# Performance work log

Measured on AMD Instinct MI355X. Metric: run time of the kernel, lower is better.

## Reference

```python
import jax, jax.numpy as jnp
import numpy as np

B, D, H, L_NS, L_S_DIM = 8, 512, 8, 64, 2048
HEAD_DIM = D // H


def setup_inputs() -> dict:
    key = jax.random.key(0)
    ks = jax.random.split(key, 12)
    L = L_S_DIM + L_NS
    x = jax.random.normal(ks[0], (B, L, D), jnp.float32)
    padding_mask = jax.random.randint(ks[1], (B, L_S_DIM), 0, 2, jnp.int32)
    s = 0.02
    params = {}
    for idx, name in enumerate(['wq', 'wk', 'wv']):
        params[name + '_sw'] = jax.random.normal(ks[2 + 3 * idx], (D, D), jnp.float32) * s
        params[name + '_sb'] = jnp.zeros((D,), jnp.float32)
        params[name + '_nw'] = jax.random.normal(ks[3 + 3 * idx], (L_NS, D, D), jnp.float32) * s
        params[name + '_nb'] = jnp.zeros((L_NS, D), jnp.float32)
    params['out_w'] = jax.random.normal(ks[11], (D, D), jnp.float32) * s
    params['out_b'] = jnp.zeros((D,), jnp.float32)
    return dict(x=x, padding_mask=padding_mask, L_s=2048, L_s_out=512, **params)


def mix_linear(x, L_s, sw, sb, nw, nb):
    # shared projection for first L_s tokens, token-specific weights for the rest
    out_s = x[:, :L_s] @ sw + sb                                # [B, L_s, D]
    out_ns = jnp.einsum('bni,nio->bno', x[:, L_s:], nw) + nb    # [B, L_ns, D]
    return jnp.concatenate([out_s, out_ns], axis=1)


def reference(x, padding_mask, L_s, L_s_out,
              wq_sw, wq_sb, wq_nw, wq_nb,
              wk_sw, wk_sb, wk_nw, wk_nb,
              wv_sw, wv_sb, wv_nw, wv_nb,
              out_w, out_b):
    Bb, L, d = x.shape
    L_ns = wq_nw.shape[0]
    hd = d // H
    K = mix_linear(x, L_s, wk_sw, wk_sb, wk_nw, wk_nb).reshape(Bb, L, H, hd).transpose(0, 2, 1, 3)
    V = mix_linear(x, L_s, wv_sw, wv_sb, wv_nw, wv_nb).reshape(Bb, L, H, hd).transpose(0, 2, 1, 3)
    if L_s_out < L_s:
        q_input = jnp.concatenate([x[:, L_s - L_s_out:L_s], x[:, L_s:]], axis=1)
    else:
        q_input = x
    L_q = L_s_out + L_ns
    L_k = L_s + L_ns
    Q = mix_linear(q_input, L_s_out, wq_sw, wq_sb, wq_nw, wq_nb).reshape(Bb, L_q, H, hd).transpose(0, 2, 1, 3)
    scores = jnp.einsum('bhqd,bhkd->bhqk', Q, K) / jnp.asarray(np.sqrt(hd), jnp.float32)
    i = jnp.arange(L_q)[:, None]
    j = jnp.arange(L_k)[None, :]
    causal = j <= i + (L_k - L_q)                                # [L_q, L_k]
    pad = jnp.concatenate([padding_mask.astype(bool), jnp.ones((Bb, L_ns), bool)], axis=1)
    mask = causal[None, None] & pad[:, None, None, :]            # [B, 1, L_q, L_k]
    scores = jnp.where(mask, scores, -1e9)
    w = jax.nn.softmax(scores, axis=-1)
    out = jnp.einsum('bhqk,bhkd->bhqd', w, V).transpose(0, 2, 1, 3).reshape(Bb, L_q, d)
    return out @ out_w + out_b
```

## Files before the change

kernel.cpp:

```cpp
#include <hip/hip_runtime.h>

typedef unsigned short u16;
typedef unsigned long long u64;
typedef short bf16x8 __attribute__((ext_vector_type(8)));
typedef float f32x4 __attribute__((ext_vector_type(4)));
typedef unsigned short u16x8 __attribute__((ext_vector_type(8)));

#define ATT_C (0.125f * 1.44269504088896340736f)

__device__ __forceinline__ u16 f2bf(float f) {
  unsigned u = __builtin_bit_cast(unsigned int, f);
  u += 0x7FFFu + ((u >> 16) & 1u);
  return (u16)(u >> 16);
}
__device__ __forceinline__ float bf2f(u16 u) {
  return __builtin_bit_cast(float, (unsigned)u << 16);
}
__device__ __forceinline__ void gload_lds16(const void* g, void* l) {
  __builtin_amdgcn_global_load_lds((__attribute__((address_space(1))) void*)(void*)g,
                                   (__attribute__((address_space(3))) void*)l, 16, 0, 0);
}

__global__ __launch_bounds__(256) void k_prep_pm(const int* __restrict__ pmask, u64* __restrict__ pbits) {
  int b = blockIdx.x;
  int t = threadIdx.x, w = t >> 6, l = t & 63;
  #pragma unroll
  for (int i = 0; i < 8; ++i) {
    int tile = i * 4 + w;
    u64 m = __ballot(pmask[b * 2048 + tile * 64 + l] != 0);
    if (l == 0) pbits[b * 32 + tile] = m;
  }
}

__global__ __launch_bounds__(256) void k_prep_x(const float* __restrict__ x, u16* __restrict__ xb) {
  int i = blockIdx.x * 256 + threadIdx.x;
  float4 v = reinterpret_cast<const float4*>(x)[i];
  ushort4 o;
  o.x = f2bf(v.x); o.y = f2bf(v.y); o.z = f2bf(v.z); o.w = f2bf(v.w);
  reinterpret_cast<ushort4*>(xb)[i] = o;
}

__global__ __launch_bounds__(256) void k_prep_wt(const float* __restrict__ w0, const float* __restrict__ w1,
                                                 const float* __restrict__ w2, const float* __restrict__ w3,
                                                 u16* __restrict__ wt) {
  __shared__ float Tl[64][65];
  int z = blockIdx.y;
  const float* W = (z == 0) ? w0 : (z == 1) ? w1 : (z == 2) ? w2 : w3;
  int kt = blockIdx.x >> 3, nt = blockIdx.x & 7;
  int t = threadIdx.x;
  int c = (t & 15) * 4, r0 = t >> 4;
  #pragma unroll
  for (int p = 0; p < 4; ++p) {
    int r = r0 + p * 16;
    float4 v = *reinterpret_cast<const float4*>(&W[(kt * 64 + r) * 512 + nt * 64 + c]);
    Tl[r][c] = v.x; Tl[r][c + 1] = v.y; Tl[r][c + 2] = v.z; Tl[r][c + 3] = v.w;
  }
  __syncthreads();
  #pragma unroll
  for (int p = 0; p < 4; ++p) {
    int n = r0 + p * 16;
    ushort4 u;
    u.x = f2bf(Tl[c + 0][n]); u.y = f2bf(Tl[c + 1][n]);
    u.z = f2bf(Tl[c + 2][n]); u.w = f2bf(Tl[c + 3][n]);
    *reinterpret_cast<ushort4*>(&wt[(z << 18) + (nt * 64 + n) * 512 + kt * 64 + c]) = u;
  }
}

__global__ __launch_bounds__(256) void k_nonshared(
    const float* __restrict__ x,
    const float* __restrict__ wq_nw, const float* __restrict__ wq_nb,
    const float* __restrict__ wk_nw, const float* __restrict__ wk_nb,
    const float* __restrict__ wv_nw, const float* __restrict__ wv_nb,
    u16* __restrict__ Qp, u16* __restrict__ Kp, u16* __restrict__ Vt) {
  int n = blockIdx.x, p = blockIdx.y;
  const float* W  = (p == 0) ? wq_nw : (p == 1) ? wk_nw : wv_nw;
  const float* bb = (p == 0) ? wq_nb : (p == 1) ? wk_nb : wv_nb;
  W += (long)n * 262144; bb += n * 512;
  __shared__ float As[4096];
  int t = threadIdx.x;
  #pragma unroll
  for (int i = 0; i < 4; ++i) {
    int f4 = t + i * 256;
    int bi = f4 >> 7;
    int off = (f4 & 127) * 4;
    reinterpret_cast<float4*>(As)[f4] =
        *reinterpret_cast<const float4*>(&x[(bi * 2112 + 2048 + n) * 512 + off]);
  }
  __syncthreads();
  int c4 = (t & 127) * 4, ih = t >> 7;
  float acc[8][4];
  #pragma unroll
  for (int b2 = 0; b2 < 8; ++b2) { acc[b2][0]=0.f; acc[b2][1]=0.f; acc[b2][2]=0.f; acc[b2][3]=0.f; }
  int i0 = ih * 256;
  #pragma unroll 8
  for (int i = i0; i < i0 + 256; ++i) {
    float4 wr = *reinterpret_cast<const float4*>(&W[i * 512 + c4]);
    #pragma unroll
    for (int b2 = 0; b2 < 8; ++b2) {
      float a = As[b2 * 512 + i];
      acc[b2][0] += a * wr.x; acc[b2][1] += a * wr.y;
      acc[b2][2] += a * wr.z; acc[b2][3] += a * wr.w;
    }
  }
  __syncthreads();
  if (ih == 1) {
    #pragma unroll
    for (int b2 = 0; b2 < 8; ++b2)
      reinterpret_cast<float4*>(As)[(t & 127) * 8 + b2] =
          make_float4(acc[b2][0], acc[b2][1], acc[b2][2], acc[b2][3]);
  }
  __syncthreads();
  if (ih == 0) {
    float4 bv = *reinterpret_cast<const float4*>(&bb[c4]);
    #pragma unroll
    for (int b2 = 0; b2 < 8; ++b2) {
      float4 o2 = reinterpret_cast<float4*>(As)[(t & 127) * 8 + b2];
      float r0 = acc[b2][0] + o2.x + bv.x, r1 = acc[b2][1] + o2.y + bv.y;
      float r2 = acc[b2][2] + o2.z + bv.z, r3 = acc[b2][3] + o2.w + bv.w;
      if (p == 0) {
        ushort4 u; u.x = f2bf(r0); u.y = f2bf(r1); u.z = f2bf(r2); u.w = f2bf(r3);
        *reinterpret_cast<ushort4*>(&Qp[(b2 * 576 + 512 + n) * 512 + c4]) = u;
      } else if (p == 1) {
        ushort4 u; u.x = f2bf(r0); u.y = f2bf(r1); u.z = f2bf(r2); u.w = f2bf(r3);
        *reinterpret_cast<ushort4*>(&Kp[(b2 * 2112 + 2048 + n) * 512 + c4]) = u;
      } else {
        Vt[(b2 * 512 + c4 + 0) * 2112 + 2048 + n] = f2bf(r0);
        Vt[(b2 * 512 + c4 + 1) * 2112 + 2048 + n] = f2bf(r1);
        Vt[(b2 * 512 + c4 + 2) * 2112 + 2048 + n] = f2bf(r2);
        Vt[(b2 * 512 + c4 + 3) * 2112 + 2048 + n] = f2bf(r3);
      }
    }
  }
}

template<int AMODE, int CMODE>
__global__ __launch_bounds__(256) void k_gemm(const u16* __restrict__ A, const u16* __restrict__ Wt,
                                              const float* __restrict__ bias, void* __restrict__ Cp,
                                              int mtpb, int arowoff, int cbs) {
  __shared__ u16 Al[4096];
  __shared__ u16 Wl[4096];
  int t = threadIdx.x, w = t >> 6, l = t & 63;
  int bm = blockIdx.x, n0 = blockIdx.y << 7;
  int batch = bm / mtpb, mt = bm % mtpb;
  int rowbase = batch * 2112 + arowoff + mt * 128;
  f32x4 zero = {0.f, 0.f, 0.f, 0.f};
  f32x4 acc[4][4];
  #pragma unroll
  for (int i = 0; i < 4; ++i)
    #pragma unroll
    for (int j = 0; j < 4; ++j) acc[i][j] = zero;
  int wm0 = (w >> 1) * 64, wn0 = (w & 1) * 64;
  int colL = l & 15, quad = l >> 4;
  for (int ks = 0; ks < 16; ++ks) {
    int k0 = ks * 32;
    #pragma unroll
    for (int hh = 0; hh < 2; ++hh) {
      int c = t + hh * 256;
      int r = c & 127, q = c >> 7;
      const u16* ga;
      if (AMODE == 0) ga = &A[(rowbase + r) * 512 + k0 + q * 8];
      else            ga = &A[((bm * 16 + ks) * 512 + c) * 8];
      gload_lds16(ga, &Al[c * 8]);
      gload_lds16(&Wt[(n0 + r) * 512 + k0 + q * 8], &Wl[c * 8]);
    }
    __syncthreads();
    bf16x8 af[4], bfr[4];
    #pragma unroll
    for (int mi = 0; mi < 4; ++mi)
      af[mi] = *reinterpret_cast<const bf16x8*>(&Al[(quad * 128 + wm0 + mi * 16 + colL) * 8]);
    #pragma unroll
    for (int ni = 0; ni < 4; ++ni)
      bfr[ni] = *reinterpret_cast<const bf16x8*>(&Wl[(quad * 128 + wn0 + ni * 16 + colL) * 8]);
    #pragma unroll
    for (int mi = 0; mi < 4; ++mi)
      #pragma unroll
      for (int ni = 0; ni < 4; ++ni)
        acc[mi][ni] = __builtin_amdgcn_mfma_f32_16x16x32_bf16(af[mi], bfr[ni], acc[mi][ni], 0, 0, 0);
    __syncthreads();
  }
  #pragma unroll
  for (int ni = 0; ni < 4; ++ni) {
    int n = n0 + wn0 + ni * 16 + colL;
    float bv = bias[n];
    #pragma unroll
    for (int mi = 0; mi < 4; ++mi) {
      int mbase = wm0 + mi * 16 + quad * 4;
      if (CMODE == 0) {
        u16* C = reinterpret_cast<u16*>(Cp);
        #pragma unroll
        for (int r = 0; r < 4; ++r)
          C[(batch * cbs + mt * 128 + mbase + r) * 512 + n] = f2bf(acc[mi][ni][r] + bv);
      } else if (CMODE == 1) {
        u16* C = reinterpret_cast<u16*>(Cp);
        int j0 = mt * 128 + mbase;
        ushort4 uv;
        uv.x = f2bf(acc[mi][ni][0] + bv); uv.y = f2bf(acc[mi][ni][1] + bv);
        uv.z = f2bf(acc[mi][ni][2] + bv); uv.w = f2bf(acc[mi][ni][3] + bv);
        *reinterpret_cast<ushort4*>(&C[(batch * 512 + n) * 2112 + j0]) = uv;
      } else {
        float* C = reinterpret_cast<float*>(Cp);
        #pragma unroll
        for (int r = 0; r < 4; ++r)
          C[(bm * 128 + mbase + r) * 512 + n] = acc[mi][ni][r] + bv;
      }
    }
  }
}

__global__ __launch_bounds__(256) void k_attn(const u16* __restrict__ Qp, const u16* __restrict__ Kp,
                                              const u16* __restrict__ Vt, const u64* __restrict__ pbits,
                                              u16* __restrict__ OPb, float* __restrict__ ML) {
  __shared__ u16 Kl[2][4096];
  __shared__ u16 Vl[2][4096];
  __shared__ u16 PL[4][1024];
  int qt = blockIdx.x, s = blockIdx.y, z = blockIdx.z;
  int b = z >> 3, h = z & 7;
  int T = qt + 25, Tq = (T + 2) / 3;
  int jt0 = s * Tq, jt1 = min(jt0 + Tq, T);
  int t = threadIdx.x, w = t >> 6, l = t & 63;
  int colL = l & 15, quad = l >> 4;
  u16* pw = PL[w];
  const u16* Kb = Kp + (b * 2112) * 512 + h * 64;
  const u16* Vb = Vt + (b * 512 + h * 64) * 2112;
  int sj0 = t >> 3, sq0 = (t & 7) ^ (sj0 & 7);
  int sj1 = (t + 256) >> 3, sq1 = ((t + 256) & 7) ^ (sj1 & 7);

  int qrow = b * 576 + qt * 64 + w * 16 + colL;
  bf16x8 qf[2];
  #pragma unroll
  for (int f = 0; f < 2; ++f)
    qf[f] = *reinterpret_cast<const bf16x8*>(&Qp[qrow * 512 + h * 64 + f * 32 + quad * 8]);
  f32x4 zero = {0.f, 0.f, 0.f, 0.f};
  f32x4 ovT[4];
  #pragma unroll
  for (int i = 0; i < 4; ++i) ovT[i] = zero;
  float m_run = -1.0e30f, l_run = 0.f;
  int i_q = qt * 64 + w * 16 + colL;

  int fidx[4][2];
  #pragma unroll
  for (int mi = 0; mi < 4; ++mi)
    #pragma unroll
    for (int f = 0; f < 2; ++f)
      fidx[mi][f] = (((mi * 16 + colL) * 8) + (((f * 4 + quad) ^ (colL & 7)))) * 8;

  {
    int jt = jt0;
    gload_lds16(&Kb[(jt * 64 + sj0) * 512 + sq0 * 8], &Kl[0][t * 8]);
    gload_lds16(&Kb[(jt * 64 + sj1) * 512 + sq1 * 8], &Kl[0][(t + 256) * 8]);
    gload_lds16(&Vb[sj0 * 2112 + jt * 64 + sq0 * 8], &Vl[0][t * 8]);
    gload_lds16(&Vb[sj1 * 2112 + jt * 64 + sq1 * 8], &Vl[0][(t + 256) * 8]);
  }
  int buf = 0;
  for (int jt = jt0; jt < jt1; ++jt) {
    __syncthreads();
    if (jt + 1 < jt1) {
      int jn = jt + 1, nb = buf ^ 1;
      gload_lds16(&Kb[(jn * 64 + sj0) * 512 + sq0 * 8], &Kl[nb][t * 8]);
      gload_lds16(&Kb[(jn * 64 + sj1) * 512 + sq1 * 8], &Kl[nb][(t + 256) * 8]);
      gload_lds16(&Vb[sj0 * 2112 + jn * 64 + sq0 * 8], &Vl[nb][t * 8]);
      gload_lds16(&Vb[sj1 * 2112 + jn * 64 + sq1 * 8], &Vl[nb][(t + 256) * 8]);
    }
    const u16* Kc = Kl[buf];
    const u16* Vc = Vl[buf];
    u64 pm = (jt < 32) ? pbits[b * 32 + jt] : ~0ULL;
    f32x4 st[4];
    #pragma unroll
    for (int mi = 0; mi < 4; ++mi) st[mi] = zero;
    #pragma unroll
    for (int mi = 0; mi < 4; ++mi)
      #pragma unroll
      for (int f = 0; f < 2; ++f) {
        bf16x8 kf = *reinterpret_cast<const bf16x8*>(&Kc[fidx[mi][f]]);
        st[mi] = __builtin_amdgcn_mfma_f32_16x16x32_bf16(kf, qf[f], st[mi], 0, 0, 0);
      }
    int thr = i_q + 1536 - jt * 64;
    float sv[4][4];
    float smax = -3.0e38f;
    #pragma unroll
    for (int mi = 0; mi < 4; ++mi)
      #pragma unroll
      for (int r = 0; r < 4; ++r) {
        int jl = mi * 16 + quad * 4 + r;
        bool ok = (jl <= thr) && (((pm >> jl) & 1ULL) != 0ULL);
        float sc = ok ? st[mi][r] : -3.0e38f;
        sv[mi][r] = sc;
        smax = fmaxf(smax, sc);
      }
    smax = fmaxf(smax, __shfl_xor(smax, 16));
    smax = fmaxf(smax, __shfl_xor(smax, 32));
    float m_new = fmaxf(m_run, smax);
    float alpha = exp2f((m_run - m_new) * ATT_C);
    float ls = 0.f;
    #pragma unroll
    for (int mi = 0; mi < 4; ++mi) {
      int o = mi * 2 + (quad >> 1);
      int jj0 = (quad & 1) * 4;
      float p0 = exp2f((sv[mi][0] - m_new) * ATT_C);
      float p1 = exp2f((sv[mi][1] - m_new) * ATT_C);
      float p2 = exp2f((sv[mi][2] - m_new) * ATT_C);
      float p3 = exp2f((sv[mi][3] - m_new) * ATT_C);
      ls += (p0 + p1) + (p2 + p3);
      u64 pk = (u64)((unsigned)f2bf(p0) | ((unsigned)f2bf(p1) << 16)) |
               ((u64)((unsigned)f2bf(p2) | ((unsigned)f2bf(p3) << 16)) << 32);
      *reinterpret_cast<u64*>(&pw[(o * 16 + colL) * 8 + jj0]) = pk;
    }
    ls += __shfl_xor(ls, 16);
    ls += __shfl_xor(ls, 32);
    l_run = l_run * alpha + ls;
    m_run = m_new;
    #pragma unroll
    for (int mi = 0; mi < 4; ++mi)
      #pragma unroll
      for (int r = 0; r < 4; ++r) ovT[mi][r] *= alpha;
    #pragma unroll
    for (int f = 0; f < 2; ++f) {
      bf16x8 pfB = *reinterpret_cast<const bf16x8*>(&pw[((f * 4 + quad) * 16 + colL) * 8]);
      #pragma unroll
      for (int mi = 0; mi < 4; ++mi) {
        bf16x8 vA = *reinterpret_cast<const bf16x8*>(&Vc[fidx[mi][f]]);
        ovT[mi] = __builtin_amdgcn_mfma_f32_16x16x32_bf16(vA, pfB, ovT[mi], 0, 0, 0);
      }
    }
    buf ^= 1;
  }
  float linv = 1.0f / l_run;
  int pid = (qt * 3 + s) * 64 + z;
  u16* op = OPb + pid * 4096;
  #pragma unroll
  for (int mi = 0; mi < 4; ++mi) {
    ushort4 uv;
    uv.x = f2bf(ovT[mi][0] * linv); uv.y = f2bf(ovT[mi][1] * linv);
    uv.z = f2bf(ovT[mi][2] * linv); uv.w = f2bf(ovT[mi][3] * linv);
    *reinterpret_cast<ushort4*>(&op[(w * 16 + colL) * 64 + mi * 16 + quad * 4]) = uv;
  }
  if (quad == 0) {
    ML[pid * 128 + w * 16 + colL] = m_run;
    ML[pid * 128 + 64 + w * 16 + colL] = l_run;
  }
}

__global__ __launch_bounds__(256) void k_attn_merge(const u16* __restrict__ OPb,
                                                    const float* __restrict__ ML,
                                                    u16* __restrict__ AO) {
  int blk = blockIdx.x;
  int qt = blk >> 6, z = blk & 63;
  int b = z >> 3, h = z & 7;
  int t = threadIdx.x;
  int q = t >> 2, g = t & 3;
  int pid0 = (qt * 3) * 64 + z;
  float m0 = ML[pid0 * 128 + q],         l0 = ML[pid0 * 128 + 64 + q];
  float m1 = ML[(pid0 + 64) * 128 + q],  l1 = ML[(pid0 + 64) * 128 + 64 + q];
  float m2 = ML[(pid0 + 128) * 128 + q], l2 = ML[(pid0 + 128) * 128 + 64 + q];
  float M = fmaxf(fmaxf(m0, m1), m2);
  float w0 = exp2f((m0 - M) * ATT_C) * l0;
  float w1 = exp2f((m1 - M) * ATT_C) * l1;
  float w2 = exp2f((m2 - M) * ATT_C) * l2;
  float rinv = 1.0f / (w0 + w1 + w2);
  w0 *= rinv; w1 *= rinv; w2 *= rinv;
  int R = b * 576 + qt * 64 + q;
  int obase = q * 64 + g * 16;
  #pragma unroll
  for (int hh = 0; hh < 2; ++hh) {
    int off = obase + hh * 8;
    u16x8 p0 = *reinterpret_cast<const u16x8*>(&OPb[pid0 * 4096 + off]);
    u16x8 p1 = *reinterpret_cast<const u16x8*>(&OPb[(pid0 + 64) * 4096 + off]);
    u16x8 p2 = *reinterpret_cast<const u16x8*>(&OPb[(pid0 + 128) * 4096 + off]);
    u16x8 o;
    #pragma unroll
    for (int i = 0; i < 8; ++i) {
      float v = bf2f(p0[i]) * w0 + bf2f(p1[i]) * w1 + bf2f(p2[i]) * w2;
      o[i] = f2bf(v);
    }
    int kk = h * 64 + g * 16 + hh * 8;
    int addr = ((((R >> 7) * 16 + (kk >> 5)) * 4 + ((kk >> 3) & 3)) << 10) + (R & 127) * 8;
    *reinterpret_cast<u16x8*>(&AO[addr]) = o;
  }
}

extern "C" void kernel_launch(void* const* d_in, const int* in_sizes, int n_in,
                              void* d_out, int out_size, void* d_ws, size_t ws_size,
                              hipStream_t stream) {
  const float* x     = (const float*)d_in[0];
  const int* pmask   = (const int*)d_in[1];
  const float* wq_sw = (const float*)d_in[4];
  const float* wq_sb = (const float*)d_in[5];
  const float* wq_nw = (const float*)d_in[6];
  const float* wq_nb = (const float*)d_in[7];
  const float* wk_sw = (const float*)d_in[8];
  const float* wk_sb = (const float*)d_in[9];
  const float* wk_nw = (const float*)d_in[10];
  const float* wk_nb = (const float*)d_in[11];
  const float* wv_sw = (const float*)d_in[12];
  const float* wv_sb = (const float*)d_in[13];
  const float* wv_nw = (const float*)d_in[14];
  const float* wv_nb = (const float*)d_in[15];
  const float* out_w = (const float*)d_in[16];
  const float* out_b = (const float*)d_in[17];

  char* ws = (char*)d_ws;
  u16* xb = (u16*)(ws);
  u16* OPb = (u16*)(ws);
  u16* wt = (u16*)(ws + 17301504);
  u16* Kp = (u16*)(ws + 19398656);
  u16* Vt = (u16*)(ws + 36700160);
  u16* Qp = (u16*)(ws + 54001664);
  u16* AO = (u16*)(ws + 58720256);
  u64* pbits = (u64*)d_out;
  float* ML = (float*)((char*)d_out + 4096);

  k_prep_pm<<<8, 256, 0, stream>>>(pmask, pbits);
  k_prep_x<<<8448, 256, 0, stream>>>(x, xb);
  k_prep_wt<<<dim3(64, 4), 256, 0, stream>>>(wq_sw, wk_sw, wv_sw, out_w, wt);
  k_nonshared<<<dim3(64, 3), 256, 0, stream>>>(x, wq_nw, wq_nb, wk_nw, wk_nb, wv_nw, wv_nb, Qp, Kp, Vt);
  k_gemm<0, 0><<<dim3(128, 4), 256, 0, stream>>>(xb, wt + 262144, wk_sb, (void*)Kp, 16, 0, 2112);
  k_gemm<0, 1><<<dim3(128, 4), 256, 0, stream>>>(xb, wt + 524288, wv_sb, (void*)Vt, 16, 0, 0);
  k_gemm<0, 0><<<dim3(32, 4), 256, 0, stream>>>(xb, wt, wq_sb, (void*)Qp, 4, 1536, 576);
  k_attn<<<dim3(9, 3, 64), 256, 0, stream>>>(Qp, Kp, Vt, pbits, OPb, ML);
  k_attn_merge<<<576, 256, 0, stream>>>(OPb, ML, AO);
  k_gemm<1, 2><<<dim3(36, 4), 256, 0, stream>>>(AO, wt + 786432, out_b, d_out, 1, 0, 0);
}
```

Baseline: 520.4 us.

## Split non-shared projection over column slices and 8-way K reduction

The per-token non-shared QKV projection kernel now launches four blocks per (token, projection), each covering 128 output columns instead of all 512. Inside a block, the 256 threads split the 512-long reduction into 8 chunks and combine the partial sums through a swizzled LDS buffer. Each thread also reads four weight rows at a time and float4 activations. The aim is more blocks in flight for this bandwidth-bound 200 MB fp32 weight stream, at the cost of extra LDS for the reduction.

```diff
diff --git a/kernel.cpp b/kernel.cpp
--- a/kernel.cpp
+++ b/kernel.cpp
@@ -72,11 +72,13 @@
     const float* __restrict__ wk_nw, const float* __restrict__ wk_nb,
     const float* __restrict__ wv_nw, const float* __restrict__ wv_nb,
     u16* __restrict__ Qp, u16* __restrict__ Kp, u16* __restrict__ Vt) {
-  int n = blockIdx.x, p = blockIdx.y;
+  int n = blockIdx.x, p = blockIdx.y, cs = blockIdx.z;
   const float* W  = (p == 0) ? wq_nw : (p == 1) ? wk_nw : wv_nw;
   const float* bb = (p == 0) ? wq_nb : (p == 1) ? wk_nb : wv_nb;
-  W += (long)n * 262144; bb += n * 512;
+  W += (long)n * 262144 + cs * 128;
+  bb += n * 512 + cs * 128;
   __shared__ float As[4096];
+  __shared__ float4 Rl4[2048];
   int t = threadIdx.x;
   #pragma unroll
   for (int i = 0; i < 4; ++i) {
@@ -87,49 +89,53 @@
         *reinterpret_cast<const float4*>(&x[(bi * 2112 + 2048 + n) * 512 + off]);
   }
   __syncthreads();
-  int c4 = (t & 127) * 4, ih = t >> 7;
+  int c4g = t & 31, ih = t >> 5;
+  int col = c4g * 4;
   float acc[8][4];
   #pragma unroll
   for (int b2 = 0; b2 < 8; ++b2) { acc[b2][0]=0.f; acc[b2][1]=0.f; acc[b2][2]=0.f; acc[b2][3]=0.f; }
-  int i0 = ih * 256;
-  #pragma unroll 8
-  for (int i = i0; i < i0 + 256; ++i) {
-    float4 wr = *reinterpret_cast<const float4*>(&W[i * 512 + c4]);
+  int r0 = ih * 64;
+  #pragma unroll 4
+  for (int ii = 0; ii < 64; ii += 4) {
+    int row = r0 + ii;
+    float4 wr0 = *reinterpret_cast<const float4*>(&W[(row + 0) * 512 + col]);
+    float4 wr1 = *reinterpret_cast<const float4*>(&W[(row + 1) * 512 + col]);
+    float4 wr2 = *reinterpret_cast<const float4*>(&W[(row + 2) * 512 + col]);
+    float4 wr3 = *reinterpret_cast<const float4*>(&W[(row + 3) * 512 + col]);
     #pragma unroll
     for (int b2 = 0; b2 < 8; ++b2) {
-      float a = As[b2 * 512 + i];
-      acc[b2][0] += a * wr.x; acc[b2][1] += a * wr.y;
-      acc[b2][2] += a * wr.z; acc[b2][3] += a * wr.w;
-    }
-  }
+      float4 a4 = *reinterpret_cast<const float4*>(&As[b2 * 512 + row]);
+      acc[b2][0] += a4.x * wr0.x + a4.y * wr1.x + a4.z * wr2.x + a4.w * wr3.x;
+      acc[b2][1] += a4.x * wr0.y + a4.y * wr1.y + a4.z * wr2.y + a4.w * wr3.y;
+      acc[b2][2] += a4.x * wr0.z + a4.y * wr1.z + a4.z * wr2.z + a4.w * wr3.z;
+      acc[b2][3] += a4.x * wr0.w + a4.y * wr1.w + a4.z * wr2.w + a4.w * wr3.w;
+    }
+  }
+  #pragma unroll
+  for (int b2 = 0; b2 < 8; ++b2)
+    Rl4[t * 8 + (b2 ^ (t & 7))] = make_float4(acc[b2][0], acc[b2][1], acc[b2][2], acc[b2][3]);
   __syncthreads();
-  if (ih == 1) {
-    #pragma unroll
-    for (int b2 = 0; b2 < 8; ++b2)
-      reinterpret_cast<float4*>(As)[(t & 127) * 8 + b2] =
-          make_float4(acc[b2][0], acc[b2][1], acc[b2][2], acc[b2][3]);
-  }
-  __syncthreads();
-  if (ih == 0) {
-    float4 bv = *reinterpret_cast<const float4*>(&bb[c4]);
-    #pragma unroll
-    for (int b2 = 0; b2 < 8; ++b2) {
-      float4 o2 = reinterpret_cast<float4*>(As)[(t & 127) * 8 + b2];
-      float r0 = acc[b2][0] + o2.x + bv.x, r1 = acc[b2][1] + o2.y + bv.y;
-      float r2 = acc[b2][2] + o2.z + bv.z, r3 = acc[b2][3] + o2.w + bv.w;
-      if (p == 0) {
-        ushort4 u; u.x = f2bf(r0); u.y = f2bf(r1); u.z = f2bf(r2); u.w = f2bf(r3);
-        *reinterpret_cast<ushort4*>(&Qp[(b2 * 576 + 512 + n) * 512 + c4]) = u;
-      } else if (p == 1) {
-        ushort4 u; u.x = f2bf(r0); u.y = f2bf(r1); u.z = f2bf(r2); u.w = f2bf(r3);
-        *reinterpret_cast<ushort4*>(&Kp[(b2 * 2112 + 2048 + n) * 512 + c4]) = u;
-      } else {
-        Vt[(b2 * 512 + c4 + 0) * 2112 + 2048 + n] = f2bf(r0);
-        Vt[(b2 * 512 + c4 + 1) * 2112 + 2048 + n] = f2bf(r1);
-        Vt[(b2 * 512 + c4 + 2) * 2112 + 2048 + n] = f2bf(r2);
-        Vt[(b2 * 512 + c4 + 3) * 2112 + 2048 + n] = f2bf(r3);
-      }
-    }
+  int oc = t >> 3, ob = t & 7;
+  float4 s = make_float4(0.f, 0.f, 0.f, 0.f);
+  #pragma unroll
+  for (int p8 = 0; p8 < 8; ++p8) {
+    float4 v = Rl4[(p8 * 32 + oc) * 8 + (ob ^ (oc & 7))];
+    s.x += v.x; s.y += v.y; s.z += v.z; s.w += v.w;
+  }
+  float4 bv = *reinterpret_cast<const float4*>(&bb[oc * 4]);
+  float q0 = s.x + bv.x, q1 = s.y + bv.y, q2 = s.z + bv.z, q3 = s.w + bv.w;
+  int gcol = cs * 128 + oc * 4;
+  if (p == 0) {
+    ushort4 u; u.x = f2bf(q0); u.y = f2bf(q1); u.z = f2bf(q2); u.w = f2bf(q3);
+    *reinterpret_cast<ushort4*>(&Qp[(ob * 576 + 512 + n) * 512 + gcol]) = u;
+  } else if (p == 1) {
+    ushort4 u; u.x = f2bf(q0); u.y = f2bf(q1); u.z = f2bf(q2); u.w = f2bf(q3);
+    *reinterpret_cast<ushort4*>(&Kp[(ob * 2112 + 2048 + n) * 512 + gcol]) = u;
+  } else {
+    Vt[(ob * 512 + gcol + 0) * 2112 + 2048 + n] = f2bf(q0);
+    Vt[(ob * 512 + gcol + 1) * 2112 + 2048 + n] = f2bf(q1);
+    Vt[(ob * 512 + gcol + 2) * 2112 + 2048 + n] = f2bf(q2);
+    Vt[(ob * 512 + gcol + 3) * 2112 + 2048 + n] = f2bf(q3);
   }
 }
 
@@ -412,7 +418,7 @@
   k_prep_pm<<<8, 256, 0, stream>>>(pmask, pbits);
   k_prep_x<<<8448, 256, 0, stream>>>(x, xb);
   k_prep_wt<<<dim3(64, 4), 256, 0, stream>>>(wq_sw, wk_sw, wv_sw, out_w, wt);
-  k_nonshared<<<dim3(64, 3), 256, 0, stream>>>(x, wq_nw, wq_nb, wk_nw, wk_nb, wv_nw, wv_nb, Qp, Kp, Vt);
+  k_nonshared<<<dim3(64, 3, 4), 256, 0, stream>>>(x, wq_nw, wq_nb, wk_nw, wk_nb, wv_nw, wv_nb, Qp, Kp, Vt);
   k_gemm<0, 0><<<dim3(128, 4), 256, 0, stream>>>(xb, wt + 262144, wk_sb, (void*)Kp, 16, 0, 2112);
   k_gemm<0, 1><<<dim3(128, 4), 256, 0, stream>>>(xb, wt + 524288, wv_sb, (void*)Vt, 16, 0, 0);
   k_gemm<0, 0><<<dim3(32, 4), 256, 0, stream>>>(xb, wt, wq_sb, (void*)Qp, 4, 1536, 576);
```

New measurement: 423.4 us. 1.23x faster.
